# Performance work log

Measured on AMD Instinct MI355X. Metric: run time of the kernel, lower is better.

The kernel has to match this reference:

```python
import jax, jax.numpy as jnp
import numpy as np

S, D, H, F = 8192, 2048, 2048, 8192
C_GATE = 8.0
EPS = 1e-6


def _rmsnorm(x, w, b):
    # eqx.nn.RMSNorm: x / sqrt(mean(x^2) + eps) * w + b, per row
    inv = jax.lax.rsqrt(jnp.mean(x * x, axis=-1, keepdims=True) + EPS)
    return x * inv * w + b


def _rglru(x, W_in, b_in, W_a, b_a, W_g, b_g, lam, W_out, b_out):
    # Real-Gated LRU (Griffin). x: [S, D] -> [S, D], hidden state size H.
    xh = x @ W_in.T + b_in                      # [S, H]
    r = jax.nn.sigmoid(x @ W_a.T + b_a)         # recurrence gate [S, H]
    g = jax.nn.sigmoid(x @ W_g.T + b_g)         # input gate      [S, H]
    log_a = C_GATE * r * jax.nn.log_sigmoid(lam)  # log a_t, a = sigmoid(lam)^(c*r)
    a = jnp.exp(log_a)                          # [S, H], in (0,1)
    b = jnp.sqrt(1.0 - jnp.exp(2.0 * log_a)) * (g * xh)

    def combine(e1, e2):
        a1, b1 = e1
        a2, b2 = e2
        return (a1 * a2, a2 * b1 + b2)

    _, h = jax.lax.associative_scan(combine, (a, b), axis=0)  # h_t = a_t h_{t-1} + b_t
    return h @ W_out.T + b_out                  # [S, D]


def _ffn(x, w1, b1, w2, b2):
    return jax.nn.gelu(x @ w1.T + b1) @ w2.T + b2


def setup_inputs() -> dict:
    key = jax.random.key(0)
    ks = jax.random.split(key, 16)
    s = 0.02  # weight init scale
    return {
        "x": jax.random.normal(ks[0], (S, D), jnp.float32),
        "W_in": jax.random.normal(ks[1], (H, D), jnp.float32) * s,
        "b_in": jnp.zeros((H,), jnp.float32),
        "W_a": jax.random.normal(ks[2], (H, D), jnp.float32) * s,
        "b_a": jnp.zeros((H,), jnp.float32),
        "W_g": jax.random.normal(ks[3], (H, D), jnp.float32) * s,
        "b_g": jnp.zeros((H,), jnp.float32),
        "lam": jax.random.normal(ks[4], (H,), jnp.float32),
        "W_out": jax.random.normal(ks[5], (D, H), jnp.float32) * s,
        "b_out": jnp.zeros((D,), jnp.float32),
        "ffn_w1": jax.random.normal(ks[6], (F, D), jnp.float32) * s,
        "ffn_b1": jnp.zeros((F,), jnp.float32),
        "ffn_w2": jax.random.normal(ks[7], (D, F), jnp.float32) * s,
        "ffn_b2": jnp.zeros((D,), jnp.float32),
        "act1_w": jax.random.normal(ks[8], (1, D), jnp.float32) * s,
        "act1_b": jnp.zeros((1,), jnp.float32),
        "act2_w": jax.random.normal(ks[9], (1, D), jnp.float32) * s,
        "act2_b": jnp.zeros((1,), jnp.float32),
        "norm1_w": jnp.ones((D,), jnp.float32),
        "norm1_b": jnp.zeros((D,), jnp.float32),
        "norm2_w": jnp.ones((D,), jnp.float32),
        "norm2_b": jnp.zeros((D,), jnp.float32),
        "u1": jax.random.uniform(ks[10], (S, 1), jnp.float32),
        "u2": jax.random.uniform(ks[11], (S, 1), jnp.float32),
    }


def reference(x, W_in, b_in, W_a, b_a, W_g, b_g, lam, W_out, b_out,
              ffn_w1, ffn_b1, ffn_w2, ffn_b2,
              act1_w, act1_b, act2_w, act2_b,
              norm1_w, norm1_b, norm2_w, norm2_b, u1, u2):
    # --- RG-LRU branch (dropout p=0 -> identity) ---
    residual = _rglru(x, W_in, b_in, W_a, b_a, W_g, b_g, lam, W_out, b_out)
    act_prob = jax.nn.sigmoid(residual @ act1_w.T + act1_b)  # [S, 1]
    act = u1 < act_prob                                      # stochastic gate
    residual = jnp.where(act, residual, 0.0)
    x = _rmsnorm(x + residual, norm1_w, norm1_b)
    # --- FFN branch ---
    residual = _ffn(x, ffn_w1, ffn_b1, ffn_w2, ffn_b2)
    act_prob = jax.nn.sigmoid(residual @ act2_w.T + act2_b)
    act = u2 < act_prob
    residual = jnp.where(act, residual, 0.0)
    x = _rmsnorm(x + residual, norm2_w, norm2_b)
    return x
```

## Files before the change

kernel.cpp:

```cpp
#include <hip/hip_runtime.h>

#define LDSW 40
#define SCAN_P 128
#define SCAN_L 64

typedef short short8 __attribute__((ext_vector_type(8)));
typedef float floatx4 __attribute__((ext_vector_type(4)));
typedef unsigned short u16;

__device__ __forceinline__ u16 bf16_rne(float v) {
    unsigned int u = __float_as_uint(v);
    u = u + 0x7fffu + ((u >> 16) & 1u);
    return (u16)(u >> 16);
}
__device__ __forceinline__ float bf16_to_f(u16 h) {
    return __uint_as_float(((unsigned int)h) << 16);
}
__device__ __forceinline__ float sigm(float x) { return 1.f / (1.f + expf(-x)); }
__device__ __forceinline__ float logsig(float x) {
    const float l = log1pf(expf(-fabsf(x)));
    return x >= 0.f ? -l : x - l;
}

__device__ __forceinline__ void cvt8(const float* p, short8& h8, short8& l8) {
    const float4 a = *(const float4*)p;
    const float4 b = *(const float4*)(p + 4);
    const float v[8] = {a.x, a.y, a.z, a.w, b.x, b.y, b.z, b.w};
#pragma unroll
    for (int j = 0; j < 8; ++j) {
        const u16 hh = bf16_rne(v[j]);
        h8[j] = (short)hh;
        l8[j] = (short)bf16_rne(v[j] - bf16_to_f(hh));
    }
}
__device__ __forceinline__ void cvt8h(const float* p, short8& h8) {
    const float4 a = *(const float4*)p;
    const float4 b = *(const float4*)(p + 4);
    const float v[8] = {a.x, a.y, a.z, a.w, b.x, b.y, b.z, b.w};
#pragma unroll
    for (int j = 0; j < 8; ++j) h8[j] = (short)bf16_rne(v[j]);
}

__device__ __forceinline__ void gld16(const u16* g, u16* l) {
    __builtin_amdgcn_global_load_lds(
        (const __attribute__((address_space(1))) void*)g,
        (__attribute__((address_space(3))) void*)l, 16, 0, 0);
}

__device__ __forceinline__ void vmwait8() { asm volatile("s_waitcnt vmcnt(8)" ::: "memory"); }
__device__ __forceinline__ void vmwait4() { asm volatile("s_waitcnt vmcnt(4)" ::: "memory"); }
__device__ __forceinline__ void vmwait0() { asm volatile("s_waitcnt vmcnt(0)" ::: "memory"); }
__device__ __forceinline__ void lgwait0() { asm volatile("s_waitcnt lgkmcnt(0)" ::: "memory"); }
__device__ __forceinline__ void barr()    { asm volatile("s_barrier" ::: "memory"); }

template <int AFMT, int NPROD, int EPI, int ACC, int ST>
__global__ __launch_bounds__(256, 2) void gemm_f32(
    const float* __restrict__ Af, const u16* __restrict__ Au,
    const float* __restrict__ Bf, const float* __restrict__ bias,
    float* C, u16* Chi, u16* Clo, const float* Q,
    long ldA, long ldB, long ldC, int K)
{
    __shared__ __align__(16) u16 sAh[128 * LDSW];
    __shared__ __align__(16) u16 sBh[128 * LDSW];
    __shared__ __align__(16) u16 sAl[NPROD == 3 ? 128 * LDSW : 8];
    __shared__ __align__(16) u16 sBl[NPROD == 3 ? 128 * LDSW : 8];

    const int tid  = threadIdx.x;
    const int lane = tid & 63;
    const int wid  = tid >> 6;
    const int wm   = (wid >> 1) << 6;
    const int wn   = (wid & 1) << 6;
    const int m16  = lane & 15;
    const int kq   = lane >> 4;
    const int koff = kq << 3;
    const long bM  = (long)blockIdx.y << 7;
    const long bN  = (long)blockIdx.x << 7;
    const int sr   = tid >> 2;
    const int sc   = (tid & 3) << 3;

    floatx4 acc[4][4] = {};

#pragma unroll 1
    for (int k0 = 0; k0 < K; k0 += 32) {
        __syncthreads();
#pragma unroll
        for (int i = 0; i < 2; ++i) {
            const int r  = sr + (i << 6);
            const int ls = r * LDSW + sc;
            if constexpr (AFMT == 0) {
                if constexpr (NPROD == 3) {
                    short8 h8, l8;
                    cvt8(Af + (bM + r) * ldA + k0 + sc, h8, l8);
                    *(short8*)&sAh[ls] = h8;
                    *(short8*)&sAl[ls] = l8;
                } else {
                    short8 h8;
                    cvt8h(Af + (bM + r) * ldA + k0 + sc, h8);
                    *(short8*)&sAh[ls] = h8;
                }
            } else {
                *(short8*)&sAh[ls] = *(const short8*)(Au + (bM + r) * ldA + k0 + sc);
            }
            if constexpr (NPROD == 3) {
                short8 h8, l8;
                cvt8(Bf + (bN + r) * ldB + k0 + sc, h8, l8);
                *(short8*)&sBh[ls] = h8;
                *(short8*)&sBl[ls] = l8;
            } else {
                short8 h8;
                cvt8h(Bf + (bN + r) * ldB + k0 + sc, h8);
                *(short8*)&sBh[ls] = h8;
            }
        }
        __syncthreads();

        short8 ah[4], bh[4];
#pragma unroll
        for (int t = 0; t < 4; ++t) {
            ah[t] = *(const short8*)&sAh[(wm + t * 16 + m16) * LDSW + koff];
            bh[t] = *(const short8*)&sBh[(wn + t * 16 + m16) * LDSW + koff];
        }
#pragma unroll
        for (int mi = 0; mi < 4; ++mi)
#pragma unroll
            for (int ni = 0; ni < 4; ++ni)
                acc[mi][ni] = __builtin_amdgcn_mfma_f32_16x16x32_bf16(ah[mi], bh[ni], acc[mi][ni], 0, 0, 0);

        if constexpr (NPROD == 3) {
            short8 al[4], bl[4];
#pragma unroll
            for (int t = 0; t < 4; ++t) {
                al[t] = *(const short8*)&sAl[(wm + t * 16 + m16) * LDSW + koff];
                bl[t] = *(const short8*)&sBl[(wn + t * 16 + m16) * LDSW + koff];
            }
#pragma unroll
            for (int mi = 0; mi < 4; ++mi)
#pragma unroll
                for (int ni = 0; ni < 4; ++ni)
                    acc[mi][ni] = __builtin_amdgcn_mfma_f32_16x16x32_bf16(ah[mi], bl[ni], acc[mi][ni], 0, 0, 0);
#pragma unroll
            for (int mi = 0; mi < 4; ++mi)
#pragma unroll
                for (int ni = 0; ni < 4; ++ni)
                    acc[mi][ni] = __builtin_amdgcn_mfma_f32_16x16x32_bf16(al[mi], bh[ni], acc[mi][ni], 0, 0, 0);
        }
    }

    float bv[4];
#pragma unroll
    for (int ni = 0; ni < 4; ++ni) bv[ni] = bias ? bias[bN + wn + ni * 16 + m16] : 0.f;

#pragma unroll
    for (int mi = 0; mi < 4; ++mi) {
#pragma unroll
        for (int ni = 0; ni < 4; ++ni) {
#pragma unroll
            for (int r = 0; r < 4; ++r) {
                const long grow = bM + wm + mi * 16 + (kq << 2) + r;
                const long gcol = bN + wn + ni * 16 + m16;
                const long idx  = grow * ldC + gcol;
                float v = acc[mi][ni][r] + bv[ni];
                if constexpr (ACC) v += C[idx];
                if constexpr (EPI == 1) v *= Q[idx];
                if constexpr (EPI == 2)
                    v = 0.5f * v * (1.f + tanhf(0.7978845608028654f * (v + 0.044715f * v * v * v)));
                if constexpr (ST == 1) {
                    const u16 h = bf16_rne(v);
                    Chi[idx] = h;
                    Clo[idx] = bf16_rne(v - bf16_to_f(h));
                } else {
                    C[idx] = v;
                }
            }
        }
    }
}

template <int NPROD, int BFMT, int EPI, int ACC, int ST, int DOT>
__global__ __launch_bounds__(256, 2) void gemm_sp(
    const u16* __restrict__ Ah, const u16* __restrict__ Al,
    const u16* __restrict__ Bh, const u16* __restrict__ Bl,
    const float* __restrict__ Bf, const float* __restrict__ bias,
    float* C, u16* Chi, const float* Q,
    const float* __restrict__ vvec, float* dacc,
    long ldA, long ldB, long ldC, int K)
{
    __shared__ __align__(16) u16 sAh[128 * 32];
    __shared__ __align__(16) u16 sBh[128 * 32];
    __shared__ __align__(16) u16 sAl[NPROD == 3 ? 128 * 32 : 8];
    __shared__ __align__(16) u16 sBl[NPROD == 3 ? 128 * 32 : 8];

    const int tid  = threadIdx.x;
    const int lane = tid & 63;
    const int wid  = tid >> 6;
    const int wm   = (wid >> 1) << 6;
    const int wn   = (wid & 1) << 6;
    const int m16  = lane & 15;
    const int kq   = lane >> 4;
    const long bM  = (long)blockIdx.y << 7;
    const long bN  = (long)blockIdx.x << 7;

    const int  drow = (wid << 5) + (lane >> 2);
    const int  qsrc = (((lane & 3) ^ ((lane >> 3) & 3)) << 3);
    const long a0   = (bM + drow) * ldA + qsrc;
    const long a1   = a0 + 16 * ldA;
    const long b0   = (bN + drow) * ldB + qsrc;
    const long b1   = b0 + 16 * ldB;
    u16* const lA0  = &sAh[(wid << 5) << 5];
    u16* const lA1  = lA0 + 512;
    u16* const lB0  = &sBh[(wid << 5) << 5];
    u16* const lB1  = lB0 + 512;
    u16* const lAl0 = &sAl[NPROD == 3 ? ((wid << 5) << 5) : 0];
    u16* const lAl1 = lAl0 + (NPROD == 3 ? 512 : 0);
    u16* const lBl0 = &sBl[NPROD == 3 ? ((wid << 5) << 5) : 0];
    u16* const lBl1 = lBl0 + (NPROD == 3 ? 512 : 0);

    const int sr  = tid >> 2;
    const int sc  = (tid & 3) << 3;
    const int wch = (((tid & 3) ^ ((sr >> 1) & 3)) << 3);

    const int kr = ((kq ^ ((m16 >> 1) & 3)) << 3);

    floatx4 acc[4][4] = {};

#pragma unroll 1
    for (int k0 = 0; k0 < K; k0 += 32) {
        __syncthreads();
        gld16(Ah + a0 + k0, lA0);
        gld16(Ah + a1 + k0, lA1);
        if constexpr (NPROD == 3) {
            gld16(Al + a0 + k0, lAl0);
            gld16(Al + a1 + k0, lAl1);
        }
        if constexpr (BFMT == 1) {
            gld16(Bh + b0 + k0, lB0);
            gld16(Bh + b1 + k0, lB1);
            if constexpr (NPROD == 3) {
                gld16(Bl + b0 + k0, lBl0);
                gld16(Bl + b1 + k0, lBl1);
            }
        } else {
#pragma unroll
            for (int i = 0; i < 2; ++i) {
                const int r = sr + (i << 6);
                short8 h8, l8;
                cvt8(Bf + (bN + r) * ldB + k0 + sc, h8, l8);
                *(short8*)&sBh[(r << 5) + wch] = h8;
                *(short8*)&sBl[(r << 5) + wch] = l8;
            }
        }
        __syncthreads();

        short8 ah[4], bh[4];
#pragma unroll
        for (int t = 0; t < 4; ++t) {
            ah[t] = *(const short8*)&sAh[((wm + t * 16 + m16) << 5) + kr];
            bh[t] = *(const short8*)&sBh[((wn + t * 16 + m16) << 5) + kr];
        }
#pragma unroll
        for (int mi = 0; mi < 4; ++mi)
#pragma unroll
            for (int ni = 0; ni < 4; ++ni)
                acc[mi][ni] = __builtin_amdgcn_mfma_f32_16x16x32_bf16(ah[mi], bh[ni], acc[mi][ni], 0, 0, 0);

        if constexpr (NPROD == 3) {
            short8 al[4], bl[4];
#pragma unroll
            for (int t = 0; t < 4; ++t) {
                al[t] = *(const short8*)&sAl[((wm + t * 16 + m16) << 5) + kr];
                bl[t] = *(const short8*)&sBl[((wn + t * 16 + m16) << 5) + kr];
            }
#pragma unroll
            for (int mi = 0; mi < 4; ++mi)
#pragma unroll
                for (int ni = 0; ni < 4; ++ni)
                    acc[mi][ni] = __builtin_amdgcn_mfma_f32_16x16x32_bf16(ah[mi], bl[ni], acc[mi][ni], 0, 0, 0);
#pragma unroll
            for (int mi = 0; mi < 4; ++mi)
#pragma unroll
                for (int ni = 0; ni < 4; ++ni)
                    acc[mi][ni] = __builtin_amdgcn_mfma_f32_16x16x32_bf16(al[mi], bh[ni], acc[mi][ni], 0, 0, 0);
        }
    }

    float bv[4];
#pragma unroll
    for (int ni = 0; ni < 4; ++ni) bv[ni] = bias ? bias[bN + wn + ni * 16 + m16] : 0.f;
    float vv[4] = {}, ls[4] = {};
    if constexpr (EPI == 3 || DOT == 1) {
#pragma unroll
        for (int ni = 0; ni < 4; ++ni) {
            vv[ni] = vvec[bN + wn + ni * 16 + m16];
            if constexpr (EPI == 3) ls[ni] = logsig(vv[ni]);
        }
    }
    float ds[4][4] = {};

#pragma unroll
    for (int mi = 0; mi < 4; ++mi) {
#pragma unroll
        for (int ni = 0; ni < 4; ++ni) {
#pragma unroll
            for (int r = 0; r < 4; ++r) {
                const long grow = bM + wm + mi * 16 + (kq << 2) + r;
                const long gcol = bN + wn + ni * 16 + m16;
                const long idx  = grow * ldC + gcol;
                float v = acc[mi][ni][r] + bv[ni];
                if constexpr (EPI == 1) v *= Q[idx];
                if constexpr (EPI == 2)
                    v = 0.5f * v * (1.f + tanhf(0.7978845608028654f * (v + 0.044715f * v * v * v)));
                if constexpr (EPI == 3) v = expf(8.f * sigm(v) * ls[ni]);
                if constexpr (EPI == 4) {
                    const float a = Q[idx];
                    v = sqrtf(fmaxf(1.f - a * a, 0.f)) * sigm(v);
                }
                if constexpr (ACC) v += C[idx];
                if constexpr (DOT) ds[mi][r] += v * vv[ni];
                if constexpr (ST == 1) Chi[idx] = bf16_rne(v);
                else C[idx] = v;
            }
        }
    }

    if constexpr (DOT) {
#pragma unroll
        for (int mi = 0; mi < 4; ++mi)
#pragma unroll
            for (int r = 0; r < 4; ++r) {
                float s = ds[mi][r];
                s += __shfl_xor(s, 1);
                s += __shfl_xor(s, 2);
                s += __shfl_xor(s, 4);
                s += __shfl_xor(s, 8);
                if (m16 == 0)
                    atomicAdd(&dacc[bM + wm + mi * 16 + (kq << 2) + r], s);
            }
    }
}

template <int NPROD, int EPI, int ACC, int ST, int DOT>
__global__ __launch_bounds__(512, 2) void gemm8(
    const u16* __restrict__ Ah, const u16* __restrict__ Al,
    const u16* __restrict__ Bh, const u16* __restrict__ Bl,
    const float* __restrict__ bias,
    float* C, u16* Chi,
    const float* __restrict__ vvec, float* dacc,
    long ldA, long ldB, long ldC, int K)
{
    constexpr int NPL = (NPROD == 3) ? 4 : 2;
    __shared__ __align__(16) u16 lds[2][NPL][8192];

    const int tid  = threadIdx.x;
    const int lane = tid & 63;
    const int wid  = tid >> 6;
    const int wr   = wid >> 2;
    const int wc   = wid & 3;
    const int m16  = lane & 15;
    const int kq   = lane >> 4;
    const long bM  = (long)blockIdx.y << 8;
    const long bN  = (long)blockIdx.x << 8;

    const int  drow = (wid << 5) + (lane >> 2);
    const int  qsrc = (((lane & 3) ^ ((lane >> 3) & 3)) << 3);
    const u16* gA0  = Ah + (bM + drow) * ldA + qsrc;
    const u16* gA1  = gA0 + (ldA << 4);
    const u16* gB0  = Bh + (bN + drow) * ldB + qsrc;
    const u16* gB1  = gB0 + (ldB << 4);
    const u16* gAl0 = (NPROD == 3 ? Al : Ah) + (bM + drow) * ldA + qsrc;
    const u16* gAl1 = gAl0 + (ldA << 4);
    const u16* gBl0 = (NPROD == 3 ? Bl : Bh) + (bN + drow) * ldB + qsrc;
    const u16* gBl1 = gBl0 + (ldB << 4);

    const int lwb = wid << 10;
    const int kr  = ((kq ^ ((m16 >> 1) & 3)) << 3);

    const int NT = K >> 5;

    auto stage = [&](int buf, int t) {
        const long k0 = (long)t << 5;
        gld16(gA0 + k0, &lds[buf][0][lwb]);
        gld16(gA1 + k0, &lds[buf][0][lwb + 512]);
        gld16(gB0 + k0, &lds[buf][1][lwb]);
        gld16(gB1 + k0, &lds[buf][1][lwb + 512]);
        if constexpr (NPROD == 3) {
            gld16(gAl0 + k0, &lds[buf][2][lwb]);
            gld16(gAl1 + k0, &lds[buf][2][lwb + 512]);
            gld16(gBl0 + k0, &lds[buf][3][lwb]);
            gld16(gBl1 + k0, &lds[buf][3][lwb + 512]);
        }
    };

    floatx4 acc[8][4] = {};
    short8 bh[4], bl[4];

    stage(0, 0);
    stage(1, 1);
    if constexpr (NPROD == 3) vmwait8(); else vmwait4();
    barr();

    const int arow = (wr << 7) + m16;
    const int brow = (wc << 6) + m16;

#pragma unroll 1
    for (int t = 0; t < NT; ++t) {
        const int p = t & 1;
#pragma unroll
        for (int q = 0; q < 4; ++q) {
            const int r0 = arow + (q << 5);
            const int r1 = r0 + 16;
            short8 ah0 = *(const short8*)&lds[p][0][(r0 << 5) + kr];
            short8 ah1 = *(const short8*)&lds[p][0][(r1 << 5) + kr];
            short8 al0 = {}, al1 = {};
            if constexpr (NPROD == 3) {
                al0 = *(const short8*)&lds[p][2][(r0 << 5) + kr];
                al1 = *(const short8*)&lds[p][2][(r1 << 5) + kr];
            }
            if (q == 0) {
#pragma unroll
                for (int ni = 0; ni < 4; ++ni) {
                    const int rb = (brow + (ni << 4)) << 5;
                    bh[ni] = *(const short8*)&lds[p][1][rb + kr];
                    if constexpr (NPROD == 3)
                        bl[ni] = *(const short8*)&lds[p][3][rb + kr];
                }
            }
            if (q < 3) {
                lgwait0();
                __builtin_amdgcn_sched_barrier(0);
                __builtin_amdgcn_s_setprio(1);
#pragma unroll
                for (int ni = 0; ni < 4; ++ni) {
                    acc[2 * q][ni]     = __builtin_amdgcn_mfma_f32_16x16x32_bf16(ah0, bh[ni], acc[2 * q][ni], 0, 0, 0);
                    acc[2 * q + 1][ni] = __builtin_amdgcn_mfma_f32_16x16x32_bf16(ah1, bh[ni], acc[2 * q + 1][ni], 0, 0, 0);
                }
                if constexpr (NPROD == 3) {
#pragma unroll
                    for (int ni = 0; ni < 4; ++ni) {
                        acc[2 * q][ni]     = __builtin_amdgcn_mfma_f32_16x16x32_bf16(ah0, bl[ni], acc[2 * q][ni], 0, 0, 0);
                        acc[2 * q + 1][ni] = __builtin_amdgcn_mfma_f32_16x16x32_bf16(ah1, bl[ni], acc[2 * q + 1][ni], 0, 0, 0);
                    }
#pragma unroll
                    for (int ni = 0; ni < 4; ++ni) {
                        acc[2 * q][ni]     = __builtin_amdgcn_mfma_f32_16x16x32_bf16(al0, bh[ni], acc[2 * q][ni], 0, 0, 0);
                        acc[2 * q + 1][ni] = __builtin_amdgcn_mfma_f32_16x16x32_bf16(al1, bh[ni], acc[2 * q + 1][ni], 0, 0, 0);
                    }
                }
                __builtin_amdgcn_s_setprio(0);
                barr();
            } else {
                lgwait0();
                barr();
                const bool pf = (t + 2 < NT);
                if (pf) stage(p, t + 2);
                __builtin_amdgcn_s_setprio(1);
#pragma unroll
                for (int ni = 0; ni < 4; ++ni) {
                    acc[6][ni] = __builtin_amdgcn_mfma_f32_16x16x32_bf16(ah0, bh[ni], acc[6][ni], 0, 0, 0);
                    acc[7][ni] = __builtin_amdgcn_mfma_f32_16x16x32_bf16(ah1, bh[ni], acc[7][ni], 0, 0, 0);
                }
                if constexpr (NPROD == 3) {
#pragma unroll
                    for (int ni = 0; ni < 4; ++ni) {
                        acc[6][ni] = __builtin_amdgcn_mfma_f32_16x16x32_bf16(ah0, bl[ni], acc[6][ni], 0, 0, 0);
                        acc[7][ni] = __builtin_amdgcn_mfma_f32_16x16x32_bf16(ah1, bl[ni], acc[7][ni], 0, 0, 0);
                    }
#pragma unroll
                    for (int ni = 0; ni < 4; ++ni) {
                        acc[6][ni] = __builtin_amdgcn_mfma_f32_16x16x32_bf16(al0, bh[ni], acc[6][ni], 0, 0, 0);
                        acc[7][ni] = __builtin_amdgcn_mfma_f32_16x16x32_bf16(al1, bh[ni], acc[7][ni], 0, 0, 0);
                    }
                }
                __builtin_amdgcn_s_setprio(0);
                if (pf) {
                    if constexpr (NPROD == 3) vmwait8(); else vmwait4();
                } else {
                    vmwait0();
                }
                barr();
            }
        }
    }

    float bv[4];
#pragma unroll
    for (int ni = 0; ni < 4; ++ni) bv[ni] = bias ? bias[bN + (wc << 6) + (ni << 4) + m16] : 0.f;
    float vv[4] = {};
    if constexpr (DOT) {
#pragma unroll
        for (int ni = 0; ni < 4; ++ni) vv[ni] = vvec[bN + (wc << 6) + (ni << 4) + m16];
    }
    float ds[8][4] = {};

#pragma unroll
    for (int mi = 0; mi < 8; ++mi) {
#pragma unroll
        for (int ni = 0; ni < 4; ++ni) {
#pragma unroll
            for (int r = 0; r < 4; ++r) {
                const long grow = bM + (wr << 7) + (mi << 4) + (kq << 2) + r;
                const long gcol = bN + (wc << 6) + (ni << 4) + m16;
                const long idx  = grow * ldC + gcol;
                float v = acc[mi][ni][r] + bv[ni];
                if constexpr (EPI == 2)
                    v = 0.5f * v * (1.f + tanhf(0.7978845608028654f * (v + 0.044715f * v * v * v)));
                if constexpr (ACC) v += C[idx];
                if constexpr (DOT) ds[mi][r] += v * vv[ni];
                if constexpr (ST == 1) Chi[idx] = bf16_rne(v);
                else C[idx] = v;
            }
        }
    }

    if constexpr (DOT) {
#pragma unroll
        for (int mi = 0; mi < 8; ++mi)
#pragma unroll
            for (int r = 0; r < 4; ++r) {
                float s = ds[mi][r];
                s += __shfl_xor(s, 1);
                s += __shfl_xor(s, 2);
                s += __shfl_xor(s, 4);
                s += __shfl_xor(s, 8);
                if (m16 == 0)
                    atomicAdd(&dacc[bM + (wr << 7) + (mi << 4) + (kq << 2) + r], s);
            }
    }
}

template <int HASLO>
__global__ __launch_bounds__(256) void split_kernel(
    const float* __restrict__ src, long lds,
    u16* __restrict__ hi, u16* __restrict__ lo, long ldd)
{
    const long r = blockIdx.x;
    const int  c = threadIdx.x << 3;
    const float* p = src + r * lds + c;
    const float4 a = *(const float4*)p;
    const float4 b = *(const float4*)(p + 4);
    const float v[8] = {a.x, a.y, a.z, a.w, b.x, b.y, b.z, b.w};
    short8 h8, l8;
#pragma unroll
    for (int j = 0; j < 8; ++j) {
        const u16 hh = bf16_rne(v[j]);
        h8[j] = (short)hh;
        if constexpr (HASLO) l8[j] = (short)bf16_rne(v[j] - bf16_to_f(hh));
    }
    *(short8*)&hi[r * ldd + c] = h8;
    if constexpr (HASLO) *(short8*)&lo[r * ldd + c] = l8;
}

__global__ __launch_bounds__(256) void zb2init_kernel(
    float* __restrict__ zb2, const float* __restrict__ zc2)
{
    zb2[blockIdx.x * 256 + threadIdx.x] = zc2[0];
}

__global__ __launch_bounds__(256) void aq_kernel(
    float* za, float* zg, const float* __restrict__ lam)
{
    const long i = ((long)blockIdx.x * 256 + threadIdx.x) * 4;
    const int  c = (int)(i & 2047);
    const float4 zav = *(const float4*)(za + i);
    const float4 zgv = *(const float4*)(zg + i);
    const float4 lmv = *(const float4*)(lam + c);
    float4 av, qv;
    const float zaa[4] = {zav.x, zav.y, zav.z, zav.w};
    const float zga[4] = {zgv.x, zgv.y, zgv.z, zgv.w};
    const float lma[4] = {lmv.x, lmv.y, lmv.z, lmv.w};
    float aa[4], qa[4];
#pragma unroll
    for (int j = 0; j < 4; ++j) {
        const float r  = sigm(zaa[j]);
        const float g  = sigm(zga[j]);
        const float la = 8.f * r * logsig(lma[j]);
        aa[j] = expf(la);
        qa[j] = sqrtf(fmaxf(1.f - expf(2.f * la), 0.f)) * g;
    }
    av.x = aa[0]; av.y = aa[1]; av.z = aa[2]; av.w = aa[3];
    qv.x = qa[0]; qv.y = qa[1]; qv.z = qa[2]; qv.w = qa[3];
    *(float4*)(za + i) = av;
    *(float4*)(zg + i) = qv;
}

__global__ __launch_bounds__(256) void scan_partial(
    const float* __restrict__ A, const float* __restrict__ B,
    float* __restrict__ Aagg, float* __restrict__ Bagg)
{
    const int c = blockIdx.x * 256 + threadIdx.x;
    const int p = blockIdx.y;
    const long base = (long)p * SCAN_L * 2048 + c;
    float Ar = 1.f, Br = 0.f;
    for (int t = 0; t < SCAN_L; ++t) {
        const float at = A[base + (long)t * 2048];
        const float bt = B[base + (long)t * 2048];
        Ar *= at;
        Br = Br * at + bt;
    }
    Aagg[p * 2048 + c] = Ar;
    Bagg[p * 2048 + c] = Br;
}

__global__ __launch_bounds__(256) void scan_combine(
    const float* __restrict__ Aagg, const float* __restrict__ Bagg,
    float* __restrict__ Hini)
{
    const int c = blockIdx.x * 256 + threadIdx.x;
    float h = 0.f;
    for (int p = 0; p < SCAN_P; ++p) {
        Hini[p * 2048 + c] = h;
        h = Aagg[p * 2048 + c] * h + Bagg[p * 2048 + c];
    }
}

__global__ __launch_bounds__(256) void scan_final(
    float* A, const float* __restrict__ B, const float* __restrict__ Hini,
    u16* __restrict__ Hhi)
{
    const int c = blockIdx.x * 256 + threadIdx.x;
    const int p = blockIdx.y;
    const long base = (long)p * SCAN_L * 2048 + c;
    float h = Hini[p * 2048 + c];
    for (int t = 0; t < SCAN_L; ++t) {
        const long idx = base + (long)t * 2048;
        h = A[idx] * h + B[idx];
        A[idx] = h;
        if (Hhi) Hhi[idx] = bf16_rne(h);
    }
}

__global__ __launch_bounds__(256) void vpart_kernel(
    const float* __restrict__ W, const float* __restrict__ w,
    float* __restrict__ part, long ldW, int dchunk)
{
    const int j  = blockIdx.x * 256 + threadIdx.x;
    const int d0 = blockIdx.y * dchunk;
    float s = 0.f;
    for (int d = 0; d < dchunk; ++d) s += W[(long)(d0 + d) * ldW + j] * w[d0 + d];
    part[(long)blockIdx.y * ldW + j] = s;
}

__global__ __launch_bounds__(256) void vreduce_kernel(
    const float* __restrict__ part, float* __restrict__ v, long ldW, int nch)
{
    const int j = blockIdx.x * 256 + threadIdx.x;
    float s = 0.f;
    for (int c = 0; c < nch; ++c) s += part[(long)c * ldW + j];
    v[j] = s;
}

__global__ __launch_bounds__(256) void dotc_kernel(
    const float* __restrict__ a, const float* __restrict__ b,
    const float* __restrict__ bias1, float* __restrict__ out)
{
    __shared__ float red[4];
    const int tid = threadIdx.x, lane = tid & 63, wid = tid >> 6;
    float s = 0.f;
    for (int d = tid; d < 2048; d += 256) s += a[d] * b[d];
#pragma unroll
    for (int off = 32; off > 0; off >>= 1) s += __shfl_down(s, off);
    if (lane == 0) red[wid] = s;
    __syncthreads();
    if (tid == 0) out[0] = red[0] + red[1] + red[2] + red[3] + bias1[0];
}

template <int INIT>
__global__ __launch_bounds__(256) void zacc_kernel(
    const u16* __restrict__ uHi, const u16* __restrict__ uLo,
    const float* __restrict__ v2s, const float* __restrict__ zc,
    float* __restrict__ zb, int L)
{
    __shared__ float red[4];
    const int tid = threadIdx.x, lane = tid & 63, wid = tid >> 6;
    const long s = blockIdx.x;
    const long base = s * (long)L;
    float dot = 0.f;
    for (int f = tid; f < L; f += 256)
        dot += (bf16_to_f(uHi[base + f]) + bf16_to_f(uLo[base + f])) * v2s[f];
#pragma unroll
    for (int off = 32; off > 0; off >>= 1) dot += __shfl_down(dot, off);
    if (lane == 0) red[wid] = dot;
    __syncthreads();
    if (tid == 0) {
        const float t = red[0] + red[1] + red[2] + red[3];
        zb[s] = INIT ? (zc[0] + t) : (zb[s] + t);
    }
}

__global__ __launch_bounds__(256) void gate1_kernel(
    const float* __restrict__ x, float* res1x1,
    const float* __restrict__ h,
    const float* __restrict__ v1, const float* __restrict__ zc1,
    const float* __restrict__ u1,
    const float* __restrict__ nw, const float* __restrict__ nb)
{
    __shared__ float red[4];
    const int tid = threadIdx.x, lane = tid & 63, wid = tid >> 6;
    const long s = blockIdx.x;
    const long base = s * 2048;

    float dot = 0.f;
#pragma unroll
    for (int k = 0; k < 8; ++k) {
        const int d = tid + (k << 8);
        dot += h[base + d] * v1[d];
    }
#pragma unroll
    for (int off = 32; off > 0; off >>= 1) dot += __shfl_down(dot, off);
    if (lane == 0) red[wid] = dot;
    __syncthreads();
    const float z = red[0] + red[1] + red[2] + red[3] + zc1[0];
    __syncthreads();

    const float g = (u1[s] < sigm(z)) ? 1.f : 0.f;

    float yv[8];
    float ss = 0.f;
#pragma unroll
    for (int k = 0; k < 8; ++k) {
        const int d = tid + (k << 8);
        const float y = x[base + d] + g * res1x1[base + d];
        yv[k] = y;
        ss += y * y;
    }
#pragma unroll
    for (int off = 32; off > 0; off >>= 1) ss += __shfl_down(ss, off);
    if (lane == 0) red[wid] = ss;
    __syncthreads();
    const float inv = rsqrtf((red[0] + red[1] + red[2] + red[3]) * (1.f / 2048.f) + 1e-6f);

#pragma unroll
    for (int k = 0; k < 8; ++k) {
        const int d = tid + (k << 8);
        res1x1[base + d] = yv[k] * inv * nw[d] + nb[d];
    }
}

__global__ __launch_bounds__(256) void gate1s_kernel(
    const float* __restrict__ x, float* res1x1,
    const float* __restrict__ h,
    const float* __restrict__ v1, const float* __restrict__ zc1,
    const float* __restrict__ u1,
    const float* __restrict__ nw, const float* __restrict__ nb)
{
    __shared__ float red[4];
    const int tid = threadIdx.x, lane = tid & 63, wid = tid >> 6;
    const long s = blockIdx.x;
    const long base = s * 2048;

    float dot = 0.f;
#pragma unroll
    for (int k = 0; k < 8; ++k) {
        const int d = tid + (k << 8);
        dot += h[base + d] * v1[d];
    }
#pragma unroll
    for (int off = 32; off > 0; off >>= 1) dot += __shfl_down(dot, off);
    if (lane == 0) red[wid] = dot;
    __syncthreads();
    const float z = red[0] + red[1] + red[2] + red[3] + zc1[0];
    __syncthreads();

    const float g = (u1[s] < sigm(z)) ? 1.f : 0.f;

    float yv[8];
    float ss = 0.f;
#pragma unroll
    for (int k = 0; k < 8; ++k) {
        const int d = tid + (k << 8);
        const float y = x[base + d] + g * res1x1[base + d];
        yv[k] = y;
        ss += y * y;
    }
#pragma unroll
    for (int off = 32; off > 0; off >>= 1) ss += __shfl_down(ss, off);
    if (lane == 0) red[wid] = ss;
    __syncthreads();
    const float inv = rsqrtf((red[0] + red[1] + red[2] + red[3]) * (1.f / 2048.f) + 1e-6f);

    u16* xs = (u16*)res1x1;
    const long sb = s * 4096;
#pragma unroll
    for (int k = 0; k < 8; ++k) {
        const int d = tid + (k << 8);
        const float o = yv[k] * inv * nw[d] + nb[d];
        const u16 hh = bf16_rne(o);
        xs[sb + d] = hh;
        xs[sb + 2048 + d] = bf16_rne(o - bf16_to_f(hh));
    }
}

__global__ __launch_bounds__(256) void gate2_kernel(
    float* x1out, const float* __restrict__ res2,
    const float* __restrict__ zb2, const float* __restrict__ u2,
    const float* __restrict__ nw, const float* __restrict__ nb)
{
    __shared__ float red[4];
    const int tid = threadIdx.x, lane = tid & 63, wid = tid >> 6;
    const long s = blockIdx.x;
    const long base = s * 2048;

    const float g = (u2[s] < sigm(zb2[s])) ? 1.f : 0.f;

    float yv[8];
    float ss = 0.f;
#pragma unroll
    for (int k = 0; k < 8; ++k) {
        const int d = tid + (k << 8);
        const float y = x1out[base + d] + g * res2[base + d];
        yv[k] = y;
        ss += y * y;
    }
#pragma unroll
    for (int off = 32; off > 0; off >>= 1) ss += __shfl_down(ss, off);
    if (lane == 0) red[wid] = ss;
    __syncthreads();
    const float inv = rsqrtf((red[0] + red[1] + red[2] + red[3]) * (1.f / 2048.f) + 1e-6f);

#pragma unroll
    for (int k = 0; k < 8; ++k) {
        const int d = tid + (k << 8);
        x1out[base + d] = yv[k] * inv * nw[d] + nb[d];
    }
}

__global__ __launch_bounds__(256) void gate2s_kernel(
    float* x1out, const float* __restrict__ res2,
    const float* __restrict__ zb2, const float* __restrict__ u2,
    const float* __restrict__ nw, const float* __restrict__ nb)
{
    __shared__ float red[4];
    const int tid = threadIdx.x, lane = tid & 63, wid = tid >> 6;
    const long s = blockIdx.x;
    const long base = s * 2048;
    const u16* xs = (const u16*)x1out;
    const long sb = s * 4096;

    const float g = (u2[s] < sigm(zb2[s])) ? 1.f : 0.f;

    float yv[8];
    float ss = 0.f;
#pragma unroll
    for (int k = 0; k < 8; ++k) {
        const int d = tid + (k << 8);
        const float x1 = bf16_to_f(xs[sb + d]) + bf16_to_f(xs[sb + 2048 + d]);
        const float y = x1 + g * res2[base + d];
        yv[k] = y;
        ss += y * y;
    }
#pragma unroll
    for (int off = 32; off > 0; off >>= 1) ss += __shfl_down(ss, off);
    if (lane == 0) red[wid] = ss;
    __syncthreads();
    const float inv = rsqrtf((red[0] + red[1] + red[2] + red[3]) * (1.f / 2048.f) + 1e-6f);

#pragma unroll
    for (int k = 0; k < 8; ++k) {
        const int d = tid + (k << 8);
        x1out[base + d] = yv[k] * inv * nw[d] + nb[d];
    }
}

extern "C" void kernel_launch(void* const* d_in, const int* in_sizes, int n_in,
                              void* d_out, int out_size, void* d_ws, size_t ws_size,
                              hipStream_t stream)
{
    const float* x     = (const float*)d_in[0];
    const float* W_in  = (const float*)d_in[1];
    const float* b_in  = (const float*)d_in[2];
    const float* W_a   = (const float*)d_in[3];
    const float* b_a   = (const float*)d_in[4];
    const float* W_g   = (const float*)d_in[5];
    const float* b_g   = (const float*)d_in[6];
    const float* lam   = (const float*)d_in[7];
    const float* W_out = (const float*)d_in[8];
    const float* b_out = (const float*)d_in[9];
    const float* w1    = (const float*)d_in[10];
    const float* fb1   = (const float*)d_in[11];
    const float* w2    = (const float*)d_in[12];
    const float* fb2   = (const float*)d_in[13];
    const float* a1w   = (const float*)d_in[14];
    const float* a1b   = (const float*)d_in[15];
    const float* a2w   = (const float*)d_in[16];
    const float* a2b   = (const float*)d_in[17];
    const float* n1w   = (const float*)d_in[18];
    const float* n1b   = (const float*)d_in[19];
    const float* n2w   = (const float*)d_in[20];
    const float* n2b   = (const float*)d_in[21];
    const float* u1    = (const float*)d_in[22];
    const float* u2    = (const float*)d_in[23];
    (void)in_sizes; (void)n_in; (void)out_size;

    float* dob = (float*)d_out;

    char* ws = (char*)d_ws;
    size_t o = 0;
    auto take = [&](size_t bytes) -> char* {
        char* p = ws + o;
        o += (bytes + 255) & ~(size_t)255;
        return p;
    };

    float* Aagg = (float*)take((size_t)SCAN_P * 2048 * 4);
    float* Bagg = (float*)take((size_t)SCAN_P * 2048 * 4);
    float* Hini = (float*)take((size_t)SCAN_P * 2048 * 4);
    float* v1   = (float*)take(2048 * 4);
    float* v2   = (float*)take(8192 * 4);
    float* vp   = (float*)take(16 * 8192 * 4);
    float* zc1  = (float*)take(256);
    float* zc2  = (float*)take(256);
    float* zb2  = (float*)take(8192 * 4);

    float* slabA = (float*)take(64ull << 20);
    const bool pathA = ws_size >= o + (64ull << 20);
    float* slabB = nullptr;
    float* res2b = nullptr;
    if (pathA) slabB = (float*)take(64ull << 20);
    else       res2b = (float*)take(16ull << 20);
    if (o > ws_size) return;

    const dim3 blk(256);

    vpart_kernel<<<dim3(8, 16), blk, 0, stream>>>(W_out, a1w, vp, 2048, 128);
    vreduce_kernel<<<8, blk, 0, stream>>>(vp, v1, 2048, 16);
    vpart_kernel<<<dim3(32, 16), blk, 0, stream>>>(w2, a2w, vp, 8192, 128);
    vreduce_kernel<<<32, blk, 0, stream>>>(vp, v2, 8192, 16);
    dotc_kernel<<<1, blk, 0, stream>>>(b_out, a1w, a1b, zc1);
    dotc_kernel<<<1, blk, 0, stream>>>(fb2, a2w, a2b, zc2);

    if (pathA) {
        u16* const xh = (u16*)slabA;
        u16* const xl = xh + (1u << 24);
        split_kernel<1><<<8192, blk, 0, stream>>>(x, 2048, xh, xl, 2048);

        gemm_sp<3, 0, 3, 0, 0, 0><<<dim3(16, 64), blk, 0, stream>>>(
            xh, xl, nullptr, nullptr, W_a, b_a, slabB, nullptr, nullptr, lam, nullptr,
            2048, 2048, 2048, 2048);
        gemm_sp<3, 0, 4, 0, 0, 0><<<dim3(16, 64), blk, 0, stream>>>(
            xh, xl, nullptr, nullptr, W_g, b_g, dob, nullptr, slabB, nullptr, nullptr,
            2048, 2048, 2048, 2048);
        gemm_sp<3, 0, 1, 0, 0, 0><<<dim3(16, 64), blk, 0, stream>>>(
            xh, xl, nullptr, nullptr, W_in, b_in, dob, nullptr, dob, nullptr, nullptr,
            2048, 2048, 2048, 2048);

        u16* const hH = (u16*)slabA;
        scan_partial<<<dim3(8, SCAN_P), blk, 0, stream>>>(slabB, dob, Aagg, Bagg);
        scan_combine<<<8, blk, 0, stream>>>(Aagg, Bagg, Hini);
        scan_final<<<dim3(8, SCAN_P), blk, 0, stream>>>(slabB, dob, Hini, hH);

        u16* const woH = hH + (1u << 24);
        split_kernel<0><<<2048, blk, 0, stream>>>(W_out, 2048, woH, nullptr, 2048);
        gemm8<1, 0, 0, 0, 0><<<dim3(8, 32), dim3(512), 0, stream>>>(
            hH, nullptr, woH, nullptr, b_out, dob, nullptr, nullptr, nullptr,
            2048, 2048, 2048, 2048);

        gate1s_kernel<<<8192, blk, 0, stream>>>(x, dob, slabB, v1, zc1, u1, n1w, n1b);

        zb2init_kernel<<<32, blk, 0, stream>>>(zb2, zc2);

        u16* const uH  = (u16*)slabA;
        u16* const w1H = uH + (1u << 24);
        u16* const w1L = w1H + (1u << 22);
        u16* const w2H = w1H + (1u << 23);
        u16* const x1h = (u16*)dob;
        for (int c = 0; c < 4; ++c) {
            const long f0 = (long)c << 11;
            split_kernel<1><<<2048, blk, 0, stream>>>(w1 + f0 * 2048, 2048, w1H, w1L, 2048);
            split_kernel<0><<<2048, blk, 0, stream>>>(w2 + f0, 8192, w2H, nullptr, 2048);
            gemm8<3, 2, 0, 1, 1><<<dim3(8, 32), dim3(512), 0, stream>>>(
                x1h, x1h + 2048, w1H, w1L, fb1 + f0, nullptr, uH,
                v2 + f0, zb2, 4096, 2048, 2048, 2048);
            if (c == 0)
                gemm8<1, 0, 0, 0, 0><<<dim3(8, 32), dim3(512), 0, stream>>>(
                    uH, nullptr, w2H, nullptr, fb2, slabB, nullptr, nullptr, nullptr,
                    2048, 2048, 2048, 2048);
            else
                gemm8<1, 0, 1, 0, 0><<<dim3(8, 32), dim3(512), 0, stream>>>(
                    uH, nullptr, w2H, nullptr, nullptr, slabB, nullptr, nullptr, nullptr,
                    2048, 2048, 2048, 2048);
        }
        gate2s_kernel<<<8192, blk, 0, stream>>>(dob, slabB, zb2, u2, n2w, n2b);
    } else {
        u16* uHi = (u16*)slabA;
        u16* uLo = uHi + (1u << 24);

        gemm_f32<0, 3, 0, 0, 0><<<dim3(16, 64), blk, 0, stream>>>(
            x, nullptr, W_a, b_a, slabA, nullptr, nullptr, nullptr, 2048, 2048, 2048, 2048);
        gemm_f32<0, 3, 0, 0, 0><<<dim3(16, 64), blk, 0, stream>>>(
            x, nullptr, W_g, b_g, dob, nullptr, nullptr, nullptr, 2048, 2048, 2048, 2048);
        aq_kernel<<<16384, blk, 0, stream>>>(slabA, dob, lam);
        gemm_f32<0, 3, 1, 0, 0><<<dim3(16, 64), blk, 0, stream>>>(
            x, nullptr, W_in, b_in, dob, nullptr, nullptr, dob, 2048, 2048, 2048, 2048);
        scan_partial<<<dim3(8, SCAN_P), blk, 0, stream>>>(slabA, dob, Aagg, Bagg);
        scan_combine<<<8, blk, 0, stream>>>(Aagg, Bagg, Hini);
        scan_final<<<dim3(8, SCAN_P), blk, 0, stream>>>(slabA, dob, Hini, nullptr);
        gemm_f32<0, 1, 0, 0, 0><<<dim3(16, 64), blk, 0, stream>>>(
            slabA, nullptr, W_out, b_out, dob, nullptr, nullptr, nullptr, 2048, 2048, 2048, 2048);
        gate1_kernel<<<8192, blk, 0, stream>>>(x, dob, slabA, v1, zc1, u1, n1w, n1b);
        for (int rb = 0; rb < 4; ++rb) {
            const long roff = (long)rb * 2048;
            gemm_f32<0, 3, 2, 0, 1><<<dim3(64, 16), blk, 0, stream>>>(
                dob + roff * 2048, nullptr, w1, fb1,
                nullptr, uHi, uLo, nullptr, 2048, 2048, 8192, 2048);
            zacc_kernel<1><<<2048, blk, 0, stream>>>(uHi, uLo, v2, zc2, zb2 + roff, 8192);
            gemm_f32<1, 1, 0, 0, 0><<<dim3(16, 16), blk, 0, stream>>>(
                nullptr, uHi, w2, fb2, res2b, nullptr, nullptr, nullptr,
                8192, 8192, 2048, 8192);
            gate2_kernel<<<2048, blk, 0, stream>>>(
                dob + roff * 2048, res2b, zb2 + roff, u2 + roff, n2w, n2b);
        }
    }
}
```

Measured before the change: 2.680 ms.

## Software-pipeline gemm8 LDS reads, stagger prefetch, swizzle blocks, use it for gate GEMMs

Rewrites the 256x256 MFMA GEMM main loop so the next A fragments are read from LDS while the current MFMAs run, and spreads the global prefetch of the next K tile across the inner steps, staggered per wave, instead of issuing it all at the last step. Adds an XCD-aware block index remap for L2 locality. The three gate/input GEMMs now run on this kernel with new fused epilogues (decay exp, sqrt gate, multiply), after pre-splitting the weights to bf16 hi/lo in a new 16MB workspace. This costs extra split kernels and register pressure, and a barrier is now taken on every inner step.

```diff
diff --git a/kernel.cpp b/kernel.cpp
--- a/kernel.cpp
+++ b/kernel.cpp
@@ -339,11 +339,11 @@
 }
 
 template <int NPROD, int EPI, int ACC, int ST, int DOT>
-__global__ __launch_bounds__(512, 2) void gemm8(
+__global__ __launch_bounds__(512, 2) void gemm8v2(
     const u16* __restrict__ Ah, const u16* __restrict__ Al,
     const u16* __restrict__ Bh, const u16* __restrict__ Bl,
     const float* __restrict__ bias,
-    float* C, u16* Chi,
+    float* C, u16* Chi, const float* __restrict__ Q,
     const float* __restrict__ vvec, float* dacc,
     long ldA, long ldB, long ldC, int K)
 {
@@ -357,8 +357,19 @@
     const int wc   = wid & 3;
     const int m16  = lane & 15;
     const int kq   = lane >> 4;
-    const long bM  = (long)blockIdx.y << 8;
-    const long bN  = (long)blockIdx.x << 8;
+    const int bst  = wid & 3;
+
+    const int nbx = gridDim.x;
+    const int lin = blockIdx.y * nbx + blockIdx.x;
+    const int nwg = nbx * gridDim.y;
+    int bx = blockIdx.x, by = blockIdx.y;
+    if ((nwg & 7) == 0) {
+        const int s = (lin & 7) * (nwg >> 3) + (lin >> 3);
+        bx = s % nbx;
+        by = s / nbx;
+    }
+    const long bM = (long)by << 8;
+    const long bN = (long)bx << 8;
 
     const int  drow = (wid << 5) + (lane >> 2);
     const int  qsrc = (((lane & 3) ^ ((lane >> 3) & 3)) << 3);
@@ -373,28 +384,33 @@
 
     const int lwb = wid << 10;
     const int kr  = ((kq ^ ((m16 >> 1) & 3)) << 3);
-
-    const int NT = K >> 5;
-
-    auto stage = [&](int buf, int t) {
+    const int NT  = K >> 5;
+
+    auto stageA = [&](int buf, int t) {
         const long k0 = (long)t << 5;
         gld16(gA0 + k0, &lds[buf][0][lwb]);
         gld16(gA1 + k0, &lds[buf][0][lwb + 512]);
+        if constexpr (NPROD == 3) {
+            gld16(gAl0 + k0, &lds[buf][2][lwb]);
+            gld16(gAl1 + k0, &lds[buf][2][lwb + 512]);
+        }
+    };
+    auto stageB = [&](int buf, int t) {
+        const long k0 = (long)t << 5;
         gld16(gB0 + k0, &lds[buf][1][lwb]);
         gld16(gB1 + k0, &lds[buf][1][lwb + 512]);
         if constexpr (NPROD == 3) {
-            gld16(gAl0 + k0, &lds[buf][2][lwb]);
-            gld16(gAl1 + k0, &lds[buf][2][lwb + 512]);
             gld16(gBl0 + k0, &lds[buf][3][lwb]);
             gld16(gBl1 + k0, &lds[buf][3][lwb + 512]);
         }
     };
 
     floatx4 acc[8][4] = {};
-    short8 bh[4], bl[4];
-
-    stage(0, 0);
-    stage(1, 1);
+    short8 bhr[4], blr[4];
+    short8 fa[2][4];
+
+    stageA(0, 0); stageB(0, 0);
+    stageA(1, 1); stageB(1, 1);
     if constexpr (NPROD == 3) vmwait8(); else vmwait4();
     barr();
 
@@ -403,91 +419,77 @@
 
 #pragma unroll 1
     for (int t = 0; t < NT; ++t) {
-        const int p = t & 1;
+        const int p  = t & 1;
+        const bool pf = (t + 2 < NT);
+
+#pragma unroll
+        for (int ni = 0; ni < 4; ++ni) {
+            const int rb = (brow + (ni << 4)) << 5;
+            bhr[ni] = *(const short8*)&lds[p][1][rb + kr];
+            if constexpr (NPROD == 3) blr[ni] = *(const short8*)&lds[p][3][rb + kr];
+        }
+        fa[0][0] = *(const short8*)&lds[p][0][(arow << 5) + kr];
+        fa[0][1] = *(const short8*)&lds[p][0][((arow + 16) << 5) + kr];
+        if constexpr (NPROD == 3) {
+            fa[0][2] = *(const short8*)&lds[p][2][(arow << 5) + kr];
+            fa[0][3] = *(const short8*)&lds[p][2][((arow + 16) << 5) + kr];
+        }
+
 #pragma unroll
         for (int q = 0; q < 4; ++q) {
-            const int r0 = arow + (q << 5);
-            const int r1 = r0 + 16;
-            short8 ah0 = *(const short8*)&lds[p][0][(r0 << 5) + kr];
-            short8 ah1 = *(const short8*)&lds[p][0][(r1 << 5) + kr];
-            short8 al0 = {}, al1 = {};
+            const int cur = q & 1;
+            const int nxt = cur ^ 1;
+            if (q < 3) {
+                const int r0 = arow + ((q + 1) << 5);
+                fa[nxt][0] = *(const short8*)&lds[p][0][(r0 << 5) + kr];
+                fa[nxt][1] = *(const short8*)&lds[p][0][((r0 + 16) << 5) + kr];
+                if constexpr (NPROD == 3) {
+                    fa[nxt][2] = *(const short8*)&lds[p][2][(r0 << 5) + kr];
+                    fa[nxt][3] = *(const short8*)&lds[p][2][((r0 + 16) << 5) + kr];
+                }
+            }
+            if (pf) {
+                if (q == 1) stageB(p, t + 2);
+                if (q == (bst >= 2 ? 3 : bst + 1)) stageA(p, t + 2);
+            }
+            __builtin_amdgcn_s_setprio(1);
+#pragma unroll
+            for (int ni = 0; ni < 4; ++ni) {
+                acc[2 * q][ni]     = __builtin_amdgcn_mfma_f32_16x16x32_bf16(fa[cur][0], bhr[ni], acc[2 * q][ni], 0, 0, 0);
+                acc[2 * q + 1][ni] = __builtin_amdgcn_mfma_f32_16x16x32_bf16(fa[cur][1], bhr[ni], acc[2 * q + 1][ni], 0, 0, 0);
+            }
             if constexpr (NPROD == 3) {
-                al0 = *(const short8*)&lds[p][2][(r0 << 5) + kr];
-                al1 = *(const short8*)&lds[p][2][(r1 << 5) + kr];
-            }
-            if (q == 0) {
 #pragma unroll
                 for (int ni = 0; ni < 4; ++ni) {
-                    const int rb = (brow + (ni << 4)) << 5;
-                    bh[ni] = *(const short8*)&lds[p][1][rb + kr];
-                    if constexpr (NPROD == 3)
-                        bl[ni] = *(const short8*)&lds[p][3][rb + kr];
+                    acc[2 * q][ni]     = __builtin_amdgcn_mfma_f32_16x16x32_bf16(fa[cur][0], blr[ni], acc[2 * q][ni], 0, 0, 0);
+                    acc[2 * q + 1][ni] = __builtin_amdgcn_mfma_f32_16x16x32_bf16(fa[cur][1], blr[ni], acc[2 * q + 1][ni], 0, 0, 0);
                 }
-            }
-            if (q < 3) {
-                lgwait0();
-                __builtin_amdgcn_sched_barrier(0);
-                __builtin_amdgcn_s_setprio(1);
 #pragma unroll
                 for (int ni = 0; ni < 4; ++ni) {
-                    acc[2 * q][ni]     = __builtin_amdgcn_mfma_f32_16x16x32_bf16(ah0, bh[ni], acc[2 * q][ni], 0, 0, 0);
-                    acc[2 * q + 1][ni] = __builtin_amdgcn_mfma_f32_16x16x32_bf16(ah1, bh[ni], acc[2 * q + 1][ni], 0, 0, 0);
+                    acc[2 * q][ni]     = __builtin_amdgcn_mfma_f32_16x16x32_bf16(fa[cur][2], bhr[ni], acc[2 * q][ni], 0, 0, 0);
+                    acc[2 * q + 1][ni] = __builtin_amdgcn_mfma_f32_16x16x32_bf16(fa[cur][3], bhr[ni], acc[2 * q + 1][ni], 0, 0, 0);
                 }
-                if constexpr (NPROD == 3) {
-#pragma unroll
-                    for (int ni = 0; ni < 4; ++ni) {
-                        acc[2 * q][ni]     = __builtin_amdgcn_mfma_f32_16x16x32_bf16(ah0, bl[ni], acc[2 * q][ni], 0, 0, 0);
-                        acc[2 * q + 1][ni] = __builtin_amdgcn_mfma_f32_16x16x32_bf16(ah1, bl[ni], acc[2 * q + 1][ni], 0, 0, 0);
-                    }
-#pragma unroll
-                    for (int ni = 0; ni < 4; ++ni) {
-                        acc[2 * q][ni]     = __builtin_amdgcn_mfma_f32_16x16x32_bf16(al0, bh[ni], acc[2 * q][ni], 0, 0, 0);
-                        acc[2 * q + 1][ni] = __builtin_amdgcn_mfma_f32_16x16x32_bf16(al1, bh[ni], acc[2 * q + 1][ni], 0, 0, 0);
-                    }
-                }
-                __builtin_amdgcn_s_setprio(0);
-                barr();
-            } else {
-                lgwait0();
-                barr();
-                const bool pf = (t + 2 < NT);
-                if (pf) stage(p, t + 2);
-                __builtin_amdgcn_s_setprio(1);
-#pragma unroll
-                for (int ni = 0; ni < 4; ++ni) {
-                    acc[6][ni] = __builtin_amdgcn_mfma_f32_16x16x32_bf16(ah0, bh[ni], acc[6][ni], 0, 0, 0);
-                    acc[7][ni] = __builtin_amdgcn_mfma_f32_16x16x32_bf16(ah1, bh[ni], acc[7][ni], 0, 0, 0);
-                }
-                if constexpr (NPROD == 3) {
-#pragma unroll
-                    for (int ni = 0; ni < 4; ++ni) {
-                        acc[6][ni] = __builtin_amdgcn_mfma_f32_16x16x32_bf16(ah0, bl[ni], acc[6][ni], 0, 0, 0);
-                        acc[7][ni] = __builtin_amdgcn_mfma_f32_16x16x32_bf16(ah1, bl[ni], acc[7][ni], 0, 0, 0);
-                    }
-#pragma unroll
-                    for (int ni = 0; ni < 4; ++ni) {
-                        acc[6][ni] = __builtin_amdgcn_mfma_f32_16x16x32_bf16(al0, bh[ni], acc[6][ni], 0, 0, 0);
-                        acc[7][ni] = __builtin_amdgcn_mfma_f32_16x16x32_bf16(al1, bh[ni], acc[7][ni], 0, 0, 0);
-                    }
-                }
-                __builtin_amdgcn_s_setprio(0);
-                if (pf) {
-                    if constexpr (NPROD == 3) vmwait8(); else vmwait4();
-                } else {
-                    vmwait0();
-                }
-                barr();
-            }
+            }
+            __builtin_amdgcn_s_setprio(0);
+            lgwait0();
+            if (q == 3) {
+                if (pf) { if constexpr (NPROD == 3) vmwait8(); else vmwait4(); }
+                else vmwait0();
+            }
+            barr();
         }
     }
 
     float bv[4];
 #pragma unroll
     for (int ni = 0; ni < 4; ++ni) bv[ni] = bias ? bias[bN + (wc << 6) + (ni << 4) + m16] : 0.f;
-    float vv[4] = {};
-    if constexpr (DOT) {
-#pragma unroll
-        for (int ni = 0; ni < 4; ++ni) vv[ni] = vvec[bN + (wc << 6) + (ni << 4) + m16];
+    float vv[4] = {}, ls[4] = {};
+    if constexpr (EPI == 3 || DOT == 1) {
+#pragma unroll
+        for (int ni = 0; ni < 4; ++ni) {
+            vv[ni] = vvec[bN + (wc << 6) + (ni << 4) + m16];
+            if constexpr (EPI == 3) ls[ni] = logsig(vv[ni]);
+        }
     }
     float ds[8][4] = {};
 
@@ -501,8 +503,14 @@
                 const long gcol = bN + (wc << 6) + (ni << 4) + m16;
                 const long idx  = grow * ldC + gcol;
                 float v = acc[mi][ni][r] + bv[ni];
+                if constexpr (EPI == 1) v *= Q[idx];
                 if constexpr (EPI == 2)
                     v = 0.5f * v * (1.f + tanhf(0.7978845608028654f * (v + 0.044715f * v * v * v)));
+                if constexpr (EPI == 3) v = expf(8.f * sigm(v) * ls[ni]);
+                if constexpr (EPI == 4) {
+                    const float a = Q[idx];
+                    v = sqrtf(fmaxf(1.f - a * a, 0.f)) * sigm(v);
+                }
                 if constexpr (ACC) v += C[idx];
                 if constexpr (DOT) ds[mi][r] += v * vv[ni];
                 if constexpr (ST == 1) Chi[idx] = bf16_rne(v);
@@ -914,11 +922,18 @@
     const bool pathA = ws_size >= o + (64ull << 20);
     float* slabB = nullptr;
     float* res2b = nullptr;
-    if (pathA) slabB = (float*)take(64ull << 20);
-    else       res2b = (float*)take(16ull << 20);
+    float* slabW = nullptr;
+    if (pathA) {
+        slabB = (float*)take(64ull << 20);
+        if (ws_size >= o + (16ull << 20)) slabW = (float*)take(16ull << 20);
+    } else {
+        res2b = (float*)take(16ull << 20);
+    }
     if (o > ws_size) return;
 
     const dim3 blk(256);
+    const dim3 blk8(512);
+    const dim3 g8(8, 32);
 
     vpart_kernel<<<dim3(8, 16), blk, 0, stream>>>(W_out, a1w, vp, 2048, 128);
     vreduce_kernel<<<8, blk, 0, stream>>>(vp, v1, 2048, 16);
@@ -932,15 +947,32 @@
         u16* const xl = xh + (1u << 24);
         split_kernel<1><<<8192, blk, 0, stream>>>(x, 2048, xh, xl, 2048);
 
-        gemm_sp<3, 0, 3, 0, 0, 0><<<dim3(16, 64), blk, 0, stream>>>(
-            xh, xl, nullptr, nullptr, W_a, b_a, slabB, nullptr, nullptr, lam, nullptr,
-            2048, 2048, 2048, 2048);
-        gemm_sp<3, 0, 4, 0, 0, 0><<<dim3(16, 64), blk, 0, stream>>>(
-            xh, xl, nullptr, nullptr, W_g, b_g, dob, nullptr, slabB, nullptr, nullptr,
-            2048, 2048, 2048, 2048);
-        gemm_sp<3, 0, 1, 0, 0, 0><<<dim3(16, 64), blk, 0, stream>>>(
-            xh, xl, nullptr, nullptr, W_in, b_in, dob, nullptr, dob, nullptr, nullptr,
-            2048, 2048, 2048, 2048);
+        if (slabW) {
+            u16* const wH = (u16*)slabW;
+            u16* const wL = wH + (1u << 22);
+            split_kernel<1><<<2048, blk, 0, stream>>>(W_a, 2048, wH, wL, 2048);
+            gemm8v2<3, 3, 0, 0, 0><<<g8, blk8, 0, stream>>>(
+                xh, xl, wH, wL, b_a, slabB, nullptr, nullptr, lam, nullptr,
+                2048, 2048, 2048, 2048);
+            split_kernel<1><<<2048, blk, 0, stream>>>(W_g, 2048, wH, wL, 2048);
+            gemm8v2<3, 4, 0, 0, 0><<<g8, blk8, 0, stream>>>(
+                xh, xl, wH, wL, b_g, dob, nullptr, slabB, nullptr, nullptr,
+                2048, 2048, 2048, 2048);
+            split_kernel<1><<<2048, blk, 0, stream>>>(W_in, 2048, wH, wL, 2048);
+            gemm8v2<3, 1, 0, 0, 0><<<g8, blk8, 0, stream>>>(
+                xh, xl, wH, wL, b_in, dob, nullptr, dob, nullptr, nullptr,
+                2048, 2048, 2048, 2048);
+        } else {
+            gemm_sp<3, 0, 3, 0, 0, 0><<<dim3(16, 64), blk, 0, stream>>>(
+                xh, xl, nullptr, nullptr, W_a, b_a, slabB, nullptr, nullptr, lam, nullptr,
+                2048, 2048, 2048, 2048);
+            gemm_sp<3, 0, 4, 0, 0, 0><<<dim3(16, 64), blk, 0, stream>>>(
+                xh, xl, nullptr, nullptr, W_g, b_g, dob, nullptr, slabB, nullptr, nullptr,
+                2048, 2048, 2048, 2048);
+            gemm_sp<3, 0, 1, 0, 0, 0><<<dim3(16, 64), blk, 0, stream>>>(
+                xh, xl, nullptr, nullptr, W_in, b_in, dob, nullptr, dob, nullptr, nullptr,
+                2048, 2048, 2048, 2048);
+        }
 
         u16* const hH = (u16*)slabA;
         scan_partial<<<dim3(8, SCAN_P), blk, 0, stream>>>(slabB, dob, Aagg, Bagg);
@@ -949,8 +981,8 @@
 
         u16* const woH = hH + (1u << 24);
         split_kernel<0><<<2048, blk, 0, stream>>>(W_out, 2048, woH, nullptr, 2048);
-        gemm8<1, 0, 0, 0, 0><<<dim3(8, 32), dim3(512), 0, stream>>>(
-            hH, nullptr, woH, nullptr, b_out, dob, nullptr, nullptr, nullptr,
+        gemm8v2<1, 0, 0, 0, 0><<<g8, blk8, 0, stream>>>(
+            hH, nullptr, woH, nullptr, b_out, dob, nullptr, nullptr, nullptr, nullptr,
             2048, 2048, 2048, 2048);
 
         gate1s_kernel<<<8192, blk, 0, stream>>>(x, dob, slabB, v1, zc1, u1, n1w, n1b);
@@ -966,16 +998,16 @@
             const long f0 = (long)c << 11;
             split_kernel<1><<<2048, blk, 0, stream>>>(w1 + f0 * 2048, 2048, w1H, w1L, 2048);
             split_kernel<0><<<2048, blk, 0, stream>>>(w2 + f0, 8192, w2H, nullptr, 2048);
-            gemm8<3, 2, 0, 1, 1><<<dim3(8, 32), dim3(512), 0, stream>>>(
-                x1h, x1h + 2048, w1H, w1L, fb1 + f0, nullptr, uH,
+            gemm8v2<3, 2, 0, 1, 1><<<g8, blk8, 0, stream>>>(
+                x1h, x1h + 2048, w1H, w1L, fb1 + f0, nullptr, uH, nullptr,
                 v2 + f0, zb2, 4096, 2048, 2048, 2048);
             if (c == 0)
-                gemm8<1, 0, 0, 0, 0><<<dim3(8, 32), dim3(512), 0, stream>>>(
-                    uH, nullptr, w2H, nullptr, fb2, slabB, nullptr, nullptr, nullptr,
+                gemm8v2<1, 0, 0, 0, 0><<<g8, blk8, 0, stream>>>(
+                    uH, nullptr, w2H, nullptr, fb2, slabB, nullptr, nullptr, nullptr, nullptr,
                     2048, 2048, 2048, 2048);
             else
-                gemm8<1, 0, 1, 0, 0><<<dim3(8, 32), dim3(512), 0, stream>>>(
-                    uH, nullptr, w2H, nullptr, nullptr, slabB, nullptr, nullptr, nullptr,
+                gemm8v2<1, 0, 1, 0, 0><<<g8, blk8, 0, stream>>>(
+                    uH, nullptr, w2H, nullptr, nullptr, slabB, nullptr, nullptr, nullptr, nullptr,
                     2048, 2048, 2048, 2048);
         }
         gate2s_kernel<<<8192, blk, 0, stream>>>(dob, slabB, zb2, u2, n2w, n2b);
```

Result: faster. 2.216 ms (-17.3%).
